# Performance work log

Measured on AMD Instinct MI355X. Metric: run time of the kernel, lower is better.

The kernel has to match this reference:

```python
import math
import jax, jax.numpy as jnp
import numpy as np

B, L, C, H = 8, 1024, 1024, 16
D = C // H  # head_dim = 64
MAX_SCALE_MUL = math.log(100.0)


def setup_inputs() -> dict:
    key = jax.random.key(0)
    ks = jax.random.split(key, 8)
    x = jax.random.normal(ks[0], (B, L, C), dtype=jnp.float32)
    # rotary frequencies: angle(l, j) = l * theta^(-2j/D), stored as (cos, sin)
    theta = 10000.0
    inv_freq = theta ** (-jnp.arange(0, D, 2, dtype=jnp.float32) / D)  # [D/2]
    ang = jnp.arange(L, dtype=jnp.float32)[:, None] * inv_freq[None, :]  # [L, D/2]
    freqs_cis = jnp.stack([jnp.cos(ang), jnp.sin(ang)], axis=-1)  # [L, D/2, 2]
    attn_bias = jnp.zeros((1, 1, L, L), dtype=jnp.float32)
    W_qkv = jax.random.normal(ks[1], (3 * C, C), dtype=jnp.float32) * (1.0 / math.sqrt(C))
    q_bias = jnp.zeros((C,), dtype=jnp.float32)
    v_bias = jnp.zeros((C,), dtype=jnp.float32)
    scale_mul_log = jnp.full((1, H, 1, 1), math.log(4.0), dtype=jnp.float32)
    W_proj = jax.random.normal(ks[2], (C, C), dtype=jnp.float32) * (1.0 / math.sqrt(C))
    b_proj = jnp.zeros((C,), dtype=jnp.float32)
    return {"x": x, "freqs_cis": freqs_cis, "attn_bias": attn_bias,
            "W_qkv": W_qkv, "q_bias": q_bias, "v_bias": v_bias,
            "scale_mul_log": scale_mul_log, "W_proj": W_proj, "b_proj": b_proj}


def _l2norm(t):
    # F.normalize(t, dim=-1): t / max(||t||_2, eps)
    n = jnp.sqrt(jnp.sum(t * t, axis=-1, keepdims=True))
    return t / jnp.maximum(n, 1e-12)


def _rope(t, fr):
    # t: [B,H,L,D]; fr: [L,D/2,2] (cos,sin). Complex mul on adjacent pairs.
    b, h, l, d = t.shape
    t2 = t.reshape(b, h, l, d // 2, 2)
    c = fr[None, None, :, :, 0]
    s = fr[None, None, :, :, 1]
    re = t2[..., 0] * c - t2[..., 1] * s
    im = t2[..., 0] * s + t2[..., 1] * c
    return jnp.stack([re, im], axis=-1).reshape(b, h, l, d)


def reference(x, freqs_cis, attn_bias, W_qkv, q_bias, v_bias, scale_mul_log, W_proj, b_proj):
    b, l, c = x.shape
    bias = jnp.concatenate([q_bias, jnp.zeros_like(q_bias), v_bias])  # [3C]
    qkv = (x @ W_qkv.T + bias).reshape(b, l, 3, H, D)
    # permute(2,0,3,1,4) -> q,k,v each [B,H,L,D]
    q = jnp.transpose(qkv[:, :, 0], (0, 2, 1, 3))
    k = jnp.transpose(qkv[:, :, 1], (0, 2, 1, 3))
    v = jnp.transpose(qkv[:, :, 2], (0, 2, 1, 3))
    # attn_l2_norm path: learned per-head scale, softmax scale = 1
    scale_mul = jnp.exp(jnp.minimum(scale_mul_log, MAX_SCALE_MUL))  # [1,H,1,1]
    q = _l2norm(q) * scale_mul
    k = _l2norm(k)
    q = _rope(q, freqs_cis)
    k = _rope(k, freqs_cis)
    scores = jnp.einsum('bhqd,bhkd->bhqk', q, k) * 1.0 + attn_bias
    attn = jax.nn.softmax(scores, axis=-1)
    out = jnp.einsum('bhqk,bhkd->bhqd', attn, v)
    out = jnp.transpose(out, (0, 2, 1, 3)).reshape(b, l, c)
    return out @ W_proj.T + b_proj
```

## Files before the change

kernel.cpp:

```cpp
#include <hip/hip_runtime.h>
#include <math.h>

#define PB 8
#define PL 1024
#define PC 1024
#define PH 16
#define PD 64
#define MAX_SCALE_MUL 4.605170185988092f
#define LOG2E 1.4426950408889634f

typedef __attribute__((ext_vector_type(8))) short s16x8;
typedef __attribute__((ext_vector_type(4))) float f32x4;

#define MFMA16(a, b, c) __builtin_amdgcn_mfma_f32_16x16x32_bf16(a, b, c, 0, 0, 0)

#if __has_builtin(__builtin_amdgcn_exp2f)
#define EXP2(x) __builtin_amdgcn_exp2f(x)
#else
#define EXP2(x) exp2f(x)
#endif

__device__ __forceinline__ unsigned short f2bf(float f) {
    unsigned u = __float_as_uint(f);
    unsigned r = (u + 0x7fffu + ((u >> 16) & 1u)) >> 16;
    return (unsigned short)r;
}

__device__ __forceinline__ unsigned pk2bf(float a, float b) {
#if __has_builtin(__builtin_amdgcn_cvt_pk_bf16_f32)
    typedef __attribute__((ext_vector_type(2))) __bf16 bf16x2_t;
    bf16x2_t r = __builtin_amdgcn_cvt_pk_bf16_f32(a, b);
    return __builtin_bit_cast(unsigned, r);
#else
    return (unsigned)f2bf(a) | ((unsigned)f2bf(b) << 16);
#endif
}

__device__ __forceinline__ void gl2lds16(const void* g, void* l) {
    __builtin_amdgcn_global_load_lds(
        (const __attribute__((address_space(1))) unsigned int*)g,
        (__attribute__((address_space(3))) unsigned int*)l, 16, 0, 0);
}

__global__ __launch_bounds__(256) void bias_flag_kernel(
    const float* __restrict__ bias, int* __restrict__ flag)
{
    int idx = blockIdx.x * 256 + threadIdx.x;
    const float4* b4 = (const float4*)bias;
    bool nz = false;
#pragma unroll
    for (int i = 0; i < 4; i++) {
        float4 v = b4[idx * 4 + i];
        nz |= (v.x != 0.f) | (v.y != 0.f) | (v.z != 0.f) | (v.w != 0.f);
    }
    if (nz) atomicOr(flag, 1);
}

__global__ __launch_bounds__(256) void cast3_kernel(
    const float* __restrict__ a, const float* __restrict__ b,
    const float* __restrict__ c,
    unsigned short* __restrict__ oa, unsigned short* __restrict__ ob,
    unsigned short* __restrict__ oc)
{
    int blk = blockIdx.x;
    const float* src; unsigned short* dst; int base;
    if (blk < 8192)       { src = a; dst = oa; base = blk; }
    else if (blk < 11264) { src = b; dst = ob; base = blk - 8192; }
    else                  { src = c; dst = oc; base = blk - 11264; }
    int i = base * 256 + threadIdx.x;
    float4 v = ((const float4*)src)[i];
    ((uint2*)dst)[i] = make_uint2(pk2bf(v.x, v.y), pk2bf(v.z, v.w));
}

__global__ __launch_bounds__(256) void gemm_qkv_lean(
    const unsigned short* __restrict__ Xh,
    const unsigned short* __restrict__ Wh,
    const float* __restrict__ qb, const float* __restrict__ vb,
    unsigned short* __restrict__ Qh, unsigned short* __restrict__ Kh,
    unsigned short* __restrict__ Vh)
{
    __shared__ unsigned short As[128 * 32];
    __shared__ unsigned short Bs[128 * 32];
    const int tid  = threadIdx.x;
    const int wave = tid >> 6, lane = tid & 63;
    const int wm = wave & 1, wn = wave >> 1;
    const int quad = lane >> 4, rr = lane & 15;
    const int m0 = blockIdx.x * 128, n0 = blockIdx.y * 128;

    f32x4 acc[4][4];
#pragma unroll
    for (int i = 0; i < 4; i++)
#pragma unroll
        for (int j = 0; j < 4; j++) acc[i][j] = (f32x4){0.f, 0.f, 0.f, 0.f};

    const int rw = lane >> 2;
    const int cc = lane & 3;
    const int g  = cc ^ ((rw >> 1) & 3);
    const int srow = wave * 32 + rw;
    const unsigned short* gA0 = Xh + (size_t)(m0 + srow) * 1024 + g * 8;
    const unsigned short* gA1 = gA0 + (size_t)16 * 1024;
    const unsigned short* gB0 = Wh + (size_t)(n0 + srow) * 1024 + g * 8;
    const unsigned short* gB1 = gB0 + (size_t)16 * 1024;
    unsigned short* lA0 = &As[(wave * 32) * 32];
    unsigned short* lA1 = &As[(wave * 32 + 16) * 32];
    unsigned short* lB0 = &Bs[(wave * 32) * 32];
    unsigned short* lB1 = &Bs[(wave * 32 + 16) * 32];

    const int swz = (rr >> 1) & 3;
    const int coff = ((quad ^ swz) * 8);

    for (int k0 = 0; k0 < 1024; k0 += 32) {
        gl2lds16(gA0, lA0); gl2lds16(gA1, lA1);
        gl2lds16(gB0, lB0); gl2lds16(gB1, lB1);
        gA0 += 32; gA1 += 32; gB0 += 32; gB1 += 32;
        __syncthreads();

        s16x8 wf[4], xf[4];
#pragma unroll
        for (int i = 0; i < 4; i++)
            wf[i] = *(const s16x8*)&Bs[(wn * 64 + i * 16 + rr) * 32 + coff];
#pragma unroll
        for (int j = 0; j < 4; j++)
            xf[j] = *(const s16x8*)&As[(wm * 64 + j * 16 + rr) * 32 + coff];
#pragma unroll
        for (int i = 0; i < 4; i++)
#pragma unroll
            for (int j = 0; j < 4; j++)
                acc[i][j] = MFMA16(wf[i], xf[j], acc[i][j]);
        __syncthreads();
    }

    const int b     = m0 >> 10;
    const int which = n0 >> 10;
    const int h     = ((n0 & 1023) + wn * 64) >> 6;
    const int lb0   = (m0 & 1023) + wm * 64;
    unsigned short* dst = (which == 0) ? Qh : ((which == 1) ? Kh : Vh);
    unsigned short* base = dst + ((size_t)(b * PH + h) * PL) * PD;
    const float* bvec = (which == 0) ? qb : vb;

#pragma unroll
    for (int i = 0; i < 4; i++) {
        const int d0 = i * 16 + quad * 4;
        float4 b4 = make_float4(0.f, 0.f, 0.f, 0.f);
        if (which != 1) b4 = *(const float4*)(bvec + h * 64 + d0);
#pragma unroll
        for (int j = 0; j < 4; j++) {
            const int l = lb0 + j * 16 + rr;
            uint2 pk = make_uint2(
                pk2bf(acc[i][j][0] + b4.x, acc[i][j][1] + b4.y),
                pk2bf(acc[i][j][2] + b4.z, acc[i][j][3] + b4.w));
            *(uint2*)(base + (size_t)l * PD + d0) = pk;
        }
    }
}

__global__ __launch_bounds__(256) void postproc_kernel(
    unsigned short* __restrict__ Qh, unsigned short* __restrict__ Kh,
    const unsigned short* __restrict__ Vh, unsigned short* __restrict__ Vt,
    const float* __restrict__ freqs, const float* __restrict__ sml)
{
    const int blk = blockIdx.x;
    const int tid = threadIdx.x;

    if (blk < 32768) {
        const bool isQ = blk < 16384;
        const int rb = isQ ? blk : blk - 16384;
        const int row = rb * 8 + (tid >> 5);
        const int li  = tid & 31;
        const int h = (row >> 10) & (PH - 1);
        const int l = row & (PL - 1);

        unsigned short* buf = isQ ? Qh : Kh;
        unsigned* p = (unsigned*)(buf + (size_t)row * PD) + li;
        unsigned v = *p;
        float v0 = __uint_as_float(v << 16);
        float v1 = __uint_as_float(v & 0xffff0000u);

        float ss = fmaf(v0, v0, v1 * v1);
#pragma unroll
        for (int off = 1; off <= 16; off <<= 1) ss += __shfl_xor(ss, off);

        float smul = isQ ? (__expf(fminf(sml[h], MAX_SCALE_MUL)) * LOG2E) : 1.0f;
        float scale = smul / fmaxf(sqrtf(ss), 1e-12f);
        v0 *= scale; v1 *= scale;

        float2 cs = ((const float2*)freqs)[l * 32 + li];
        float re = v0 * cs.x - v1 * cs.y;
        float im = fmaf(v0, cs.y, v1 * cs.x);
        *p = pk2bf(re, im);
        return;
    }

    const int vblk = blk - 32768;
    const int bh = vblk >> 4;
    const int l0 = (vblk & 15) * 64;
#pragma unroll
    for (int s = 0; s < 2; s++) {
        int slot = s * 256 + tid;
        int d  = slot & 63;
        int lb = l0 + (slot >> 6) * 8;
        unsigned o[4];
#pragma unroll
        for (int i = 0; i < 4; i++) {
            unsigned short a0 = Vh[((size_t)bh * PL + lb + 2 * i) * PD + d];
            unsigned short a1 = Vh[((size_t)bh * PL + lb + 2 * i + 1) * PD + d];
            o[i] = (unsigned)a0 | ((unsigned)a1 << 16);
        }
        *(uint4*)&Vt[((size_t)bh * PD + d) * PL + lb] = make_uint4(o[0], o[1], o[2], o[3]);
    }
}

__global__ __launch_bounds__(256) void attn_mfma(
    const unsigned short* __restrict__ Qh, const unsigned short* __restrict__ Kh,
    const unsigned short* __restrict__ Vt, const float* __restrict__ bias,
    const float* __restrict__ sml, const int* __restrict__ biasflag,
    unsigned short* __restrict__ O)
{
    __shared__ unsigned short Ks[64 * 64];
    __shared__ unsigned short Vs[64 * 64];
    __shared__ unsigned int   Ps[4][16 * 36];

    const int tid  = threadIdx.x;
    const int wave = tid >> 6, lane = tid & 63;
    const int quad = lane >> 4, rr = lane & 15;
    const int bh = blockIdx.x, q0 = blockIdx.y * 128;
    const int b = bh >> 4, h = bh & 15;
    const int hasbias = *biasflag;

    const float M = __expf(fminf(sml[h], MAX_SCALE_MUL)) * LOG2E;
    const f32x4 negM = (f32x4){-M, -M, -M, -M};

    const int sr = wave * 16 + (lane >> 3);
    const int sc = lane & 7;
    const int sg = sc ^ (sr & 7);
    const int swz8 = rr & 7;

    const size_t kvbase = (size_t)bh * PL * PD;

    s16x8 qB[2][2];
#pragma unroll
    for (int g = 0; g < 2; g++) {
        const size_t qrow = (size_t)bh * PL + q0 + g * 64 + wave * 16 + rr;
        qB[g][0] = *(const s16x8*)(Qh + qrow * PD + quad * 8);
        qB[g][1] = *(const s16x8*)(Qh + qrow * PD + 32 + quad * 8);
    }

    f32x4 accO[2][4];
#pragma unroll
    for (int g = 0; g < 2; g++)
#pragma unroll
        for (int jd = 0; jd < 4; jd++) accO[g][jd] = (f32x4){0.f, 0.f, 0.f, 0.f};
    float lsum[2] = {0.f, 0.f};

    for (int kb = 0; kb < 16; kb++) {
        gl2lds16(Kh + kvbase + (size_t)(kb * 64 + sr) * PD + sg * 8, &Ks[(wave * 16) * 64]);
        gl2lds16(Kh + kvbase + (size_t)(kb * 64 + sr + 8) * PD + sg * 8, &Ks[(wave * 16 + 8) * 64]);
        gl2lds16(Vt + kvbase + (size_t)sr * PL + kb * 64 + sg * 8, &Vs[(wave * 16) * 64]);
        gl2lds16(Vt + kvbase + (size_t)(sr + 8) * PL + kb * 64 + sg * 8, &Vs[(wave * 16 + 8) * 64]);
        __syncthreads();

        s16x8 kA[4][2];
#pragma unroll
        for (int s = 0; s < 4; s++) {
            kA[s][0] = *(const s16x8*)&Ks[(s * 16 + rr) * 64 + ((0 + quad) ^ swz8) * 8];
            kA[s][1] = *(const s16x8*)&Ks[(s * 16 + rr) * 64 + ((4 + quad) ^ swz8) * 8];
        }
        f32x4 sc4[2][4];
#pragma unroll
        for (int g = 0; g < 2; g++)
#pragma unroll
            for (int s = 0; s < 4; s++) {
                f32x4 z = MFMA16(kA[s][0], qB[g][0], negM);
                z = MFMA16(kA[s][1], qB[g][1], z);
                sc4[g][s] = z;
            }

        if (hasbias) {
#pragma unroll
            for (int g = 0; g < 2; g++) {
                const float* brow = bias + (size_t)(q0 + g * 64 + wave * 16 + rr) * PL + kb * 64;
#pragma unroll
                for (int s = 0; s < 4; s++) {
                    float4 bv = *(const float4*)(brow + s * 16 + quad * 4);
                    sc4[g][s][0] = fmaf(bv.x, LOG2E, sc4[g][s][0]);
                    sc4[g][s][1] = fmaf(bv.y, LOG2E, sc4[g][s][1]);
                    sc4[g][s][2] = fmaf(bv.z, LOG2E, sc4[g][s][2]);
                    sc4[g][s][3] = fmaf(bv.w, LOG2E, sc4[g][s][3]);
                }
            }
        }

#pragma unroll
        for (int g = 0; g < 2; g++)
#pragma unroll
            for (int s = 0; s < 4; s++) {
                sc4[g][s][0] = EXP2(sc4[g][s][0]);
                sc4[g][s][1] = EXP2(sc4[g][s][1]);
                sc4[g][s][2] = EXP2(sc4[g][s][2]);
                sc4[g][s][3] = EXP2(sc4[g][s][3]);
                lsum[g] += sc4[g][s][0] + sc4[g][s][1] + sc4[g][s][2] + sc4[g][s][3];
            }

        s16x8 vA[4][2];
#pragma unroll
        for (int s = 0; s < 4; s++) {
            vA[s][0] = *(const s16x8*)&Vs[(s * 16 + rr) * 64 + ((0 + quad) ^ swz8) * 8];
            vA[s][1] = *(const s16x8*)&Vs[(s * 16 + rr) * 64 + ((4 + quad) ^ swz8) * 8];
        }
#pragma unroll
        for (int g = 0; g < 2; g++) {
#pragma unroll
            for (int s = 0; s < 4; s++) {
                *(uint2*)&Ps[wave][rr * 36 + s * 8 + quad * 2] =
                    make_uint2(pk2bf(sc4[g][s][0], sc4[g][s][1]),
                               pk2bf(sc4[g][s][2], sc4[g][s][3]));
            }
            s16x8 pB0 = *(const s16x8*)&Ps[wave][rr * 36 + quad * 4];
            s16x8 pB1 = *(const s16x8*)&Ps[wave][rr * 36 + 16 + quad * 4];
#pragma unroll
            for (int jd = 0; jd < 4; jd++) {
                accO[g][jd] = MFMA16(vA[jd][0], pB0, accO[g][jd]);
                accO[g][jd] = MFMA16(vA[jd][1], pB1, accO[g][jd]);
            }
        }
        __syncthreads();
    }

    const int lr = lane >> 2, cch = lane & 3;
#pragma unroll
    for (int g = 0; g < 2; g++) {
        float ls = lsum[g];
        ls += __shfl_xor(ls, 16);
        ls += __shfl_xor(ls, 32);
        float inv = 1.0f / ls;
#pragma unroll
        for (int jd = 0; jd < 4; jd++) {
            *(uint2*)&Ps[wave][rr * 36 + jd * 8 + quad * 2] =
                make_uint2(pk2bf(accO[g][jd][0] * inv, accO[g][jd][1] * inv),
                           pk2bf(accO[g][jd][2] * inv, accO[g][jd][3] * inv));
        }
        uint4 w0 = *(const uint4*)&Ps[wave][lr * 36 + cch * 8];
        uint4 w1 = *(const uint4*)&Ps[wave][lr * 36 + cch * 8 + 4];
        size_t ob = ((size_t)(b * PL + q0 + g * 64 + wave * 16 + lr) * PC + h * PD);
        *(uint4*)(O + ob + cch * 16)     = w0;
        *(uint4*)(O + ob + cch * 16 + 8) = w1;
    }
}

__global__ __launch_bounds__(256) void gemm_proj_mfma(
    const unsigned short* __restrict__ Ah,
    const unsigned short* __restrict__ Wh,
    const float* __restrict__ bp, float* __restrict__ Out)
{
    __shared__ unsigned short As[128 * 32];
    __shared__ unsigned short Bs[128 * 32];
    const int tid  = threadIdx.x;
    const int wave = tid >> 6, lane = tid & 63;
    const int wm = wave & 1, wn = wave >> 1;
    const int quad = lane >> 4, rr = lane & 15;
    const int m0 = blockIdx.x * 128, n0 = blockIdx.y * 128;

    f32x4 acc[4][4];
#pragma unroll
    for (int i = 0; i < 4; i++)
#pragma unroll
        for (int j = 0; j < 4; j++) acc[i][j] = (f32x4){0.f, 0.f, 0.f, 0.f};

    const int rw = lane >> 2;
    const int cc = lane & 3;
    const int g  = cc ^ ((rw >> 1) & 3);
    const int srow = wave * 32 + rw;
    const unsigned short* gA0 = Ah + (size_t)(m0 + srow) * 1024 + g * 8;
    const unsigned short* gA1 = gA0 + (size_t)16 * 1024;
    const unsigned short* gB0 = Wh + (size_t)(n0 + srow) * 1024 + g * 8;
    const unsigned short* gB1 = gB0 + (size_t)16 * 1024;
    unsigned short* lA0 = &As[(wave * 32) * 32];
    unsigned short* lA1 = &As[(wave * 32 + 16) * 32];
    unsigned short* lB0 = &Bs[(wave * 32) * 32];
    unsigned short* lB1 = &Bs[(wave * 32 + 16) * 32];

    const int swz = (rr >> 1) & 3;
    const int coff = ((quad ^ swz) * 8);

    for (int k0 = 0; k0 < 1024; k0 += 32) {
        gl2lds16(gA0, lA0); gl2lds16(gA1, lA1);
        gl2lds16(gB0, lB0); gl2lds16(gB1, lB1);
        gA0 += 32; gA1 += 32; gB0 += 32; gB1 += 32;
        __syncthreads();

        s16x8 af[4], bf[4];
#pragma unroll
        for (int i = 0; i < 4; i++)
            af[i] = *(const s16x8*)&As[(wm * 64 + i * 16 + rr) * 32 + coff];
#pragma unroll
        for (int j = 0; j < 4; j++)
            bf[j] = *(const s16x8*)&Bs[(wn * 64 + j * 16 + rr) * 32 + coff];
#pragma unroll
        for (int i = 0; i < 4; i++)
#pragma unroll
            for (int j = 0; j < 4; j++)
                acc[i][j] = MFMA16(af[i], bf[j], acc[i][j]);
        __syncthreads();
    }

#pragma unroll
    for (int i = 0; i < 4; i++) {
        const int mb = m0 + wm * 64 + i * 16 + quad * 4;
#pragma unroll
        for (int j = 0; j < 4; j++) {
            const int n = n0 + wn * 64 + j * 16 + rr;
            const float bb = bp[n];
#pragma unroll
            for (int reg = 0; reg < 4; reg++)
                Out[(size_t)(mb + reg) * 1024 + n] = acc[i][j][reg] + bb;
        }
    }
}

extern "C" void kernel_launch(void* const* d_in, const int* in_sizes, int n_in,
                              void* d_out, int out_size, void* d_ws, size_t ws_size,
                              hipStream_t stream)
{
    const float* x         = (const float*)d_in[0];
    const float* freqs     = (const float*)d_in[1];
    const float* attn_bias = (const float*)d_in[2];
    const float* W_qkv     = (const float*)d_in[3];
    const float* q_bias    = (const float*)d_in[4];
    const float* v_bias    = (const float*)d_in[5];
    const float* sml       = (const float*)d_in[6];
    const float* W_proj    = (const float*)d_in[7];
    const float* b_proj    = (const float*)d_in[8];
    float* out = (float*)d_out;

    unsigned char* w = (unsigned char*)d_ws;
    const size_t MB = 1ull << 20;
    unsigned short* xh  = (unsigned short*)(w + 0);
    unsigned short* wqh = (unsigned short*)(w + 16 * MB);
    unsigned short* wph = (unsigned short*)(w + 22 * MB);
    unsigned short* Qh  = (unsigned short*)(w + 24 * MB);
    unsigned short* Kh  = (unsigned short*)(w + 40 * MB);
    unsigned short* Vh  = (unsigned short*)(w + 56 * MB);
    unsigned short* Vt  = (unsigned short*)(w + 72 * MB);
    unsigned short* Oh  = (unsigned short*)(w + 88 * MB);
    int*            flg = (int*)(w + 104 * MB);

    hipMemsetAsync(flg, 0, sizeof(int), stream);
    bias_flag_kernel<<<256, 256, 0, stream>>>(attn_bias, flg);
    cast3_kernel<<<12288, 256, 0, stream>>>(x, W_qkv, W_proj, xh, wqh, wph);
    gemm_qkv_lean<<<dim3(64, 24), 256, 0, stream>>>(xh, wqh, q_bias, v_bias, Qh, Kh, Vh);
    postproc_kernel<<<34816, 256, 0, stream>>>(Qh, Kh, Vh, Vt, freqs, sml);
    attn_mfma<<<dim3(128, 8), 256, 0, stream>>>(Qh, Kh, Vt, attn_bias, sml, flg, Oh);
    gemm_proj_mfma<<<dim3(64, 8), 256, 0, stream>>>(Oh, wph, b_proj, out);
}
```

Baseline: 292.0 us.

## Fuse Q norm/RoPE into attention, merge bias check, widen GEMM K-tile

Folds the attention-bias nonzero check into the cast kernel as extra blocks, which saves one launch. Q L2-normalisation, per-head scaling and RoPE move into the attention kernel's Q-fragment load, so postproc only handles K and the V transpose. Both GEMMs now stage a 64-wide K slice per iteration with an 8-way XOR swizzle, halving the number of barriers. The projection epilogue now writes float4 vectors. The cost is double the LDS per GEMM block and some extra ALU work in the attention prologue.

After: 282.6 us. 1.03x faster.

```diff
diff --git a/kernel.cpp b/kernel.cpp
--- a/kernel.cpp
+++ b/kernel.cpp
@@ -42,27 +42,25 @@
         (__attribute__((address_space(3))) unsigned int*)l, 16, 0, 0);
 }
 
-__global__ __launch_bounds__(256) void bias_flag_kernel(
-    const float* __restrict__ bias, int* __restrict__ flag)
-{
-    int idx = blockIdx.x * 256 + threadIdx.x;
-    const float4* b4 = (const float4*)bias;
-    bool nz = false;
-#pragma unroll
-    for (int i = 0; i < 4; i++) {
-        float4 v = b4[idx * 4 + i];
-        nz |= (v.x != 0.f) | (v.y != 0.f) | (v.z != 0.f) | (v.w != 0.f);
-    }
-    if (nz) atomicOr(flag, 1);
-}
-
-__global__ __launch_bounds__(256) void cast3_kernel(
+__global__ __launch_bounds__(256) void cast3f_kernel(
     const float* __restrict__ a, const float* __restrict__ b,
-    const float* __restrict__ c,
+    const float* __restrict__ c, const float* __restrict__ bias,
     unsigned short* __restrict__ oa, unsigned short* __restrict__ ob,
-    unsigned short* __restrict__ oc)
+    unsigned short* __restrict__ oc, int* __restrict__ flag)
 {
     int blk = blockIdx.x;
+    if (blk >= 12288) {
+        int idx = (blk - 12288) * 256 + threadIdx.x;
+        const float4* b4 = (const float4*)bias;
+        bool nz = false;
+#pragma unroll
+        for (int i = 0; i < 4; i++) {
+            float4 v = b4[idx * 4 + i];
+            nz |= (v.x != 0.f) | (v.y != 0.f) | (v.z != 0.f) | (v.w != 0.f);
+        }
+        if (nz) atomicOr(flag, 1);
+        return;
+    }
     const float* src; unsigned short* dst; int base;
     if (blk < 8192)       { src = a; dst = oa; base = blk; }
     else if (blk < 11264) { src = b; dst = ob; base = blk - 8192; }
@@ -79,8 +77,8 @@
     unsigned short* __restrict__ Qh, unsigned short* __restrict__ Kh,
     unsigned short* __restrict__ Vh)
 {
-    __shared__ unsigned short As[128 * 32];
-    __shared__ unsigned short Bs[128 * 32];
+    __shared__ unsigned short As[128 * 64];
+    __shared__ unsigned short Bs[128 * 64];
     const int tid  = threadIdx.x;
     const int wave = tid >> 6, lane = tid & 63;
     const int wm = wave & 1, wn = wave >> 1;
@@ -93,40 +91,41 @@
 #pragma unroll
         for (int j = 0; j < 4; j++) acc[i][j] = (f32x4){0.f, 0.f, 0.f, 0.f};
 
-    const int rw = lane >> 2;
-    const int cc = lane & 3;
-    const int g  = cc ^ ((rw >> 1) & 3);
-    const int srow = wave * 32 + rw;
-    const unsigned short* gA0 = Xh + (size_t)(m0 + srow) * 1024 + g * 8;
-    const unsigned short* gA1 = gA0 + (size_t)16 * 1024;
-    const unsigned short* gB0 = Wh + (size_t)(n0 + srow) * 1024 + g * 8;
-    const unsigned short* gB1 = gB0 + (size_t)16 * 1024;
-    unsigned short* lA0 = &As[(wave * 32) * 32];
-    unsigned short* lA1 = &As[(wave * 32 + 16) * 32];
-    unsigned short* lB0 = &Bs[(wave * 32) * 32];
-    unsigned short* lB1 = &Bs[(wave * 32 + 16) * 32];
-
-    const int swz = (rr >> 1) & 3;
-    const int coff = ((quad ^ swz) * 8);
-
-    for (int k0 = 0; k0 < 1024; k0 += 32) {
-        gl2lds16(gA0, lA0); gl2lds16(gA1, lA1);
-        gl2lds16(gB0, lB0); gl2lds16(gB1, lB1);
-        gA0 += 32; gA1 += 32; gB0 += 32; gB1 += 32;
-        __syncthreads();
-
-        s16x8 wf[4], xf[4];
-#pragma unroll
-        for (int i = 0; i < 4; i++)
-            wf[i] = *(const s16x8*)&Bs[(wn * 64 + i * 16 + rr) * 32 + coff];
-#pragma unroll
-        for (int j = 0; j < 4; j++)
-            xf[j] = *(const s16x8*)&As[(wm * 64 + j * 16 + rr) * 32 + coff];
-#pragma unroll
-        for (int i = 0; i < 4; i++)
+    const int r8 = lane >> 3;
+    const int c8 = lane & 7;
+    const int g  = c8 ^ r8;
+    const unsigned short* gA = Xh + (size_t)(m0 + wave * 32 + r8) * 1024 + g * 8;
+    const unsigned short* gB = Wh + (size_t)(n0 + wave * 32 + r8) * 1024 + g * 8;
+    unsigned short* lA = &As[(wave * 32) * 64];
+    unsigned short* lB = &Bs[(wave * 32) * 64];
+
+    const int swz8 = rr & 7;
+
+    for (int k0 = 0; k0 < 16; k0++) {
+#pragma unroll
+        for (int t = 0; t < 4; t++) {
+            gl2lds16(gA + (size_t)t * 8192, &lA[(t * 8) * 64]);
+            gl2lds16(gB + (size_t)t * 8192, &lB[(t * 8) * 64]);
+        }
+        gA += 64; gB += 64;
+        __syncthreads();
+
+#pragma unroll
+        for (int kk = 0; kk < 2; kk++) {
+            const int coff = ((kk * 4 + quad) ^ swz8) * 8;
+            s16x8 wf[4], xf[4];
+#pragma unroll
+            for (int i = 0; i < 4; i++)
+                wf[i] = *(const s16x8*)&Bs[(wn * 64 + i * 16 + rr) * 64 + coff];
 #pragma unroll
             for (int j = 0; j < 4; j++)
-                acc[i][j] = MFMA16(wf[i], xf[j], acc[i][j]);
+                xf[j] = *(const s16x8*)&As[(wm * 64 + j * 16 + rr) * 64 + coff];
+#pragma unroll
+            for (int i = 0; i < 4; i++)
+#pragma unroll
+                for (int j = 0; j < 4; j++)
+                    acc[i][j] = MFMA16(wf[i], xf[j], acc[i][j]);
+        }
         __syncthreads();
     }
 
@@ -155,23 +154,19 @@
 }
 
 __global__ __launch_bounds__(256) void postproc_kernel(
-    unsigned short* __restrict__ Qh, unsigned short* __restrict__ Kh,
+    unsigned short* __restrict__ Kh,
     const unsigned short* __restrict__ Vh, unsigned short* __restrict__ Vt,
-    const float* __restrict__ freqs, const float* __restrict__ sml)
+    const float* __restrict__ freqs)
 {
     const int blk = blockIdx.x;
     const int tid = threadIdx.x;
 
-    if (blk < 32768) {
-        const bool isQ = blk < 16384;
-        const int rb = isQ ? blk : blk - 16384;
-        const int row = rb * 8 + (tid >> 5);
+    if (blk < 16384) {
+        const int row = blk * 8 + (tid >> 5);
         const int li  = tid & 31;
-        const int h = (row >> 10) & (PH - 1);
         const int l = row & (PL - 1);
 
-        unsigned short* buf = isQ ? Qh : Kh;
-        unsigned* p = (unsigned*)(buf + (size_t)row * PD) + li;
+        unsigned* p = (unsigned*)(Kh + (size_t)row * PD) + li;
         unsigned v = *p;
         float v0 = __uint_as_float(v << 16);
         float v1 = __uint_as_float(v & 0xffff0000u);
@@ -180,8 +175,7 @@
 #pragma unroll
         for (int off = 1; off <= 16; off <<= 1) ss += __shfl_xor(ss, off);
 
-        float smul = isQ ? (__expf(fminf(sml[h], MAX_SCALE_MUL)) * LOG2E) : 1.0f;
-        float scale = smul / fmaxf(sqrtf(ss), 1e-12f);
+        float scale = 1.0f / fmaxf(sqrtf(ss), 1e-12f);
         v0 *= scale; v1 *= scale;
 
         float2 cs = ((const float2*)freqs)[l * 32 + li];
@@ -191,7 +185,7 @@
         return;
     }
 
-    const int vblk = blk - 32768;
+    const int vblk = blk - 16384;
     const int bh = vblk >> 4;
     const int l0 = (vblk & 15) * 64;
 #pragma unroll
@@ -214,7 +208,7 @@
     const unsigned short* __restrict__ Qh, const unsigned short* __restrict__ Kh,
     const unsigned short* __restrict__ Vt, const float* __restrict__ bias,
     const float* __restrict__ sml, const int* __restrict__ biasflag,
-    unsigned short* __restrict__ O)
+    const float* __restrict__ freqs, unsigned short* __restrict__ O)
 {
     __shared__ unsigned short Ks[64 * 64];
     __shared__ unsigned short Vs[64 * 64];
@@ -236,13 +230,41 @@
     const int swz8 = rr & 7;
 
     const size_t kvbase = (size_t)bh * PL * PD;
+    const float2* fr2 = (const float2*)freqs;
 
     s16x8 qB[2][2];
 #pragma unroll
     for (int g = 0; g < 2; g++) {
-        const size_t qrow = (size_t)bh * PL + q0 + g * 64 + wave * 16 + rr;
-        qB[g][0] = *(const s16x8*)(Qh + qrow * PD + quad * 8);
-        qB[g][1] = *(const s16x8*)(Qh + qrow * PD + 32 + quad * 8);
+        const int ql = q0 + g * 64 + wave * 16 + rr;
+        const size_t qoff = ((size_t)bh * PL + ql) * PD;
+        uint4 r0 = *(const uint4*)(Qh + qoff + quad * 8);
+        uint4 r1 = *(const uint4*)(Qh + qoff + 32 + quad * 8);
+        unsigned uu[8] = {r0.x, r0.y, r0.z, r0.w, r1.x, r1.y, r1.z, r1.w};
+        float lo[8], hi[8];
+        float ss = 0.f;
+#pragma unroll
+        for (int m = 0; m < 8; m++) {
+            lo[m] = __uint_as_float(uu[m] << 16);
+            hi[m] = __uint_as_float(uu[m] & 0xffff0000u);
+            ss = fmaf(lo[m], lo[m], fmaf(hi[m], hi[m], ss));
+        }
+        ss += __shfl_xor(ss, 16);
+        ss += __shfl_xor(ss, 32);
+        const float scale = M / fmaxf(sqrtf(ss), 1e-12f);
+        unsigned outw[8];
+#pragma unroll
+        for (int m = 0; m < 8; m++) {
+            const int idx = (m >> 2) * 16 + quad * 4 + (m & 3);
+            float2 cs = fr2[(size_t)ql * 32 + idx];
+            float av = lo[m] * scale, bv = hi[m] * scale;
+            float re = av * cs.x - bv * cs.y;
+            float im = fmaf(av, cs.y, bv * cs.x);
+            outw[m] = pk2bf(re, im);
+        }
+        uint4 w0 = make_uint4(outw[0], outw[1], outw[2], outw[3]);
+        uint4 w1 = make_uint4(outw[4], outw[5], outw[6], outw[7]);
+        qB[g][0] = __builtin_bit_cast(s16x8, w0);
+        qB[g][1] = __builtin_bit_cast(s16x8, w1);
     }
 
     f32x4 accO[2][4];
@@ -352,8 +374,8 @@
     const unsigned short* __restrict__ Wh,
     const float* __restrict__ bp, float* __restrict__ Out)
 {
-    __shared__ unsigned short As[128 * 32];
-    __shared__ unsigned short Bs[128 * 32];
+    __shared__ unsigned short As[128 * 64];
+    __shared__ unsigned short Bs[128 * 64];
     const int tid  = threadIdx.x;
     const int wave = tid >> 6, lane = tid & 63;
     const int wm = wave & 1, wn = wave >> 1;
@@ -366,53 +388,54 @@
 #pragma unroll
         for (int j = 0; j < 4; j++) acc[i][j] = (f32x4){0.f, 0.f, 0.f, 0.f};
 
-    const int rw = lane >> 2;
-    const int cc = lane & 3;
-    const int g  = cc ^ ((rw >> 1) & 3);
-    const int srow = wave * 32 + rw;
-    const unsigned short* gA0 = Ah + (size_t)(m0 + srow) * 1024 + g * 8;
-    const unsigned short* gA1 = gA0 + (size_t)16 * 1024;
-    const unsigned short* gB0 = Wh + (size_t)(n0 + srow) * 1024 + g * 8;
-    const unsigned short* gB1 = gB0 + (size_t)16 * 1024;
-    unsigned short* lA0 = &As[(wave * 32) * 32];
-    unsigned short* lA1 = &As[(wave * 32 + 16) * 32];
-    unsigned short* lB0 = &Bs[(wave * 32) * 32];
-    unsigned short* lB1 = &Bs[(wave * 32 + 16) * 32];
-
-    const int swz = (rr >> 1) & 3;
-    const int coff = ((quad ^ swz) * 8);
-
-    for (int k0 = 0; k0 < 1024; k0 += 32) {
-        gl2lds16(gA0, lA0); gl2lds16(gA1, lA1);
-        gl2lds16(gB0, lB0); gl2lds16(gB1, lB1);
-        gA0 += 32; gA1 += 32; gB0 += 32; gB1 += 32;
-        __syncthreads();
-
-        s16x8 af[4], bf[4];
-#pragma unroll
-        for (int i = 0; i < 4; i++)
-            af[i] = *(const s16x8*)&As[(wm * 64 + i * 16 + rr) * 32 + coff];
-#pragma unroll
-        for (int j = 0; j < 4; j++)
-            bf[j] = *(const s16x8*)&Bs[(wn * 64 + j * 16 + rr) * 32 + coff];
-#pragma unroll
-        for (int i = 0; i < 4; i++)
+    const int r8 = lane >> 3;
+    const int c8 = lane & 7;
+    const int g  = c8 ^ r8;
+    const unsigned short* gA = Ah + (size_t)(m0 + wave * 32 + r8) * 1024 + g * 8;
+    const unsigned short* gB = Wh + (size_t)(n0 + wave * 32 + r8) * 1024 + g * 8;
+    unsigned short* lA = &As[(wave * 32) * 64];
+    unsigned short* lB = &Bs[(wave * 32) * 64];
+
+    const int swz8 = rr & 7;
+
+    for (int k0 = 0; k0 < 16; k0++) {
+#pragma unroll
+        for (int t = 0; t < 4; t++) {
+            gl2lds16(gA + (size_t)t * 8192, &lA[(t * 8) * 64]);
+            gl2lds16(gB + (size_t)t * 8192, &lB[(t * 8) * 64]);
+        }
+        gA += 64; gB += 64;
+        __syncthreads();
+
+#pragma unroll
+        for (int kk = 0; kk < 2; kk++) {
+            const int coff = ((kk * 4 + quad) ^ swz8) * 8;
+            s16x8 wf[4], xf[4];
+#pragma unroll
+            for (int i = 0; i < 4; i++)
+                wf[i] = *(const s16x8*)&Bs[(wn * 64 + i * 16 + rr) * 64 + coff];
 #pragma unroll
             for (int j = 0; j < 4; j++)
-                acc[i][j] = MFMA16(af[i], bf[j], acc[i][j]);
+                xf[j] = *(const s16x8*)&As[(wm * 64 + j * 16 + rr) * 64 + coff];
+#pragma unroll
+            for (int i = 0; i < 4; i++)
+#pragma unroll
+                for (int j = 0; j < 4; j++)
+                    acc[i][j] = MFMA16(wf[i], xf[j], acc[i][j]);
+        }
         __syncthreads();
     }
 
 #pragma unroll
     for (int i = 0; i < 4; i++) {
-        const int mb = m0 + wm * 64 + i * 16 + quad * 4;
+        const int nn = n0 + wn * 64 + i * 16 + quad * 4;
+        const float4 bb = *(const float4*)(bp + nn);
 #pragma unroll
         for (int j = 0; j < 4; j++) {
-            const int n = n0 + wn * 64 + j * 16 + rr;
-            const float bb = bp[n];
-#pragma unroll
-            for (int reg = 0; reg < 4; reg++)
-                Out[(size_t)(mb + reg) * 1024 + n] = acc[i][j][reg] + bb;
+            const int m = m0 + wm * 64 + j * 16 + rr;
+            float4 o = make_float4(acc[i][j][0] + bb.x, acc[i][j][1] + bb.y,
+                                   acc[i][j][2] + bb.z, acc[i][j][3] + bb.w);
+            *(float4*)(Out + (size_t)m * 1024 + nn) = o;
         }
     }
 }
@@ -445,10 +468,10 @@
     int*            flg = (int*)(w + 104 * MB);
 
     hipMemsetAsync(flg, 0, sizeof(int), stream);
-    bias_flag_kernel<<<256, 256, 0, stream>>>(attn_bias, flg);
-    cast3_kernel<<<12288, 256, 0, stream>>>(x, W_qkv, W_proj, xh, wqh, wph);
+    cast3f_kernel<<<12544, 256, 0, stream>>>(x, W_qkv, W_proj, attn_bias,
+                                             xh, wqh, wph, flg);
     gemm_qkv_lean<<<dim3(64, 24), 256, 0, stream>>>(xh, wqh, q_bias, v_bias, Qh, Kh, Vh);
-    postproc_kernel<<<34816, 256, 0, stream>>>(Qh, Kh, Vh, Vt, freqs, sml);
-    attn_mfma<<<dim3(128, 8), 256, 0, stream>>>(Qh, Kh, Vt, attn_bias, sml, flg, Oh);
+    postproc_kernel<<<18432, 256, 0, stream>>>(Kh, Vh, Vt, freqs);
+    attn_mfma<<<dim3(128, 8), 256, 0, stream>>>(Qh, Kh, Vt, attn_bias, sml, flg, freqs, Oh);
     gemm_proj_mfma<<<dim3(64, 8), 256, 0, stream>>>(Oh, wph, b_proj, out);
 }
```
